# Kernel tuning notes

Measured on AMD Instinct MI355X. Metric: run time of the kernel, lower is better.

## Reference

```python
import jax, jax.numpy as jnp
import numpy as np

N_NODES = 100000
N_GRAPHS = 64
EPS = 1e-5


def _sage_conv(x, src, dst, Wl, bl, Wr):
    # mean-aggregate neighbor messages (src -> dst), then lin_l(agg) + lin_r(x)
    n = x.shape[0]
    deg = jax.ops.segment_sum(jnp.ones_like(dst, dtype=x.dtype), dst, num_segments=n)
    agg = jax.ops.segment_sum(x[src], dst, num_segments=n)  # [N, d]
    agg = agg / jnp.maximum(deg, 1.0)[:, None]
    return agg @ Wl + bl + x @ Wr


def _bn_relu(x, gamma, beta):
    mu = jnp.mean(x, axis=0)
    var = jnp.var(x, axis=0)
    return jax.nn.relu((x - mu) * jax.lax.rsqrt(var + EPS) * gamma + beta)


def setup_inputs() -> dict:
    key = jax.random.key(0)
    ks = jax.random.split(key, 16)
    E = 1600000
    x = jax.random.normal(ks[0], (N_NODES, 2), dtype=jnp.float32)
    edge_index = jax.random.randint(ks[1], (2, E), 0, N_NODES, dtype=jnp.int64)
    batch = jnp.sort(jax.random.randint(ks[2], (N_NODES,), 0, N_GRAPHS, dtype=jnp.int64))

    def lin(k, din, dout):
        s = 1.0 / np.sqrt(din)
        return jax.random.uniform(k, (din, dout), jnp.float32, -s, s)

    d = {"x": x, "edge_index": edge_index, "batch": batch}
    dims = [(2, 32), (32, 64), (64, 128)]
    for i, (din, dout) in enumerate(dims, 1):
        k1, k2 = jax.random.split(ks[2 + i])
        d[f"Wl{i}"] = lin(k1, din, dout)
        d[f"bl{i}"] = jnp.zeros((dout,), jnp.float32)
        d[f"Wr{i}"] = lin(k2, din, dout)
        d[f"g{i}"] = jnp.ones((dout,), jnp.float32)
        d[f"be{i}"] = jnp.zeros((dout,), jnp.float32)
    d["Wf1"] = lin(ks[10], 128, 64)
    d["bf1"] = jnp.zeros((64,), jnp.float32)
    d["Wf2"] = lin(ks[11], 64, 1)
    d["bf2"] = jnp.zeros((1,), jnp.float32)
    return d


def reference(x, edge_index, batch,
              Wl1, bl1, Wr1, g1, be1,
              Wl2, bl2, Wr2, g2, be2,
              Wl3, bl3, Wr3, g3, be3,
              Wf1, bf1, Wf2, bf2):
    src, dst = edge_index[0], edge_index[1]
    h = _bn_relu(_sage_conv(x, src, dst, Wl1, bl1, Wr1), g1, be1)
    h = _bn_relu(_sage_conv(h, src, dst, Wl2, bl2, Wr2), g2, be2)
    h = _bn_relu(_sage_conv(h, src, dst, Wl3, bl3, Wr3), g3, be3)
    # global mean pool over graphs
    cnt = jax.ops.segment_sum(jnp.ones_like(batch, dtype=h.dtype), batch, num_segments=N_GRAPHS)
    pooled = jax.ops.segment_sum(h, batch, num_segments=N_GRAPHS) / jnp.maximum(cnt, 1.0)[:, None]
    out = jax.nn.relu(pooled @ Wf1 + bf1)
    # dropout is identity in eval mode
    return out @ Wf2 + bf2
```

## Files before the change

### kernel.cpp

```cpp
#include <hip/hip_runtime.h>
#include <hip/hip_fp16.h>

#define N_NODES 100000
#define N_GRAPHS 64
#define BN_EPS 1e-5

#define NB 782
#define NC 49
#define PT1 4096
#define PT2 2048
#define BPC 16
#define CAP 3072
#define CAPC 36864
#define CAPF 3072

typedef _Float16 f16x8 __attribute__((ext_vector_type(8)));
typedef float f32x4 __attribute__((ext_vector_type(4)));

union F16x8u {
    f16x8 v;
    __half2 h2[4];
    uint4 u;
};

__device__ __forceinline__ float bfly64(float v) {
#pragma unroll
    for (int m = 1; m < 64; m <<= 1) v += __shfl_xor(v, m, 64);
    return v;
}

__device__ __forceinline__ unsigned pack_h2(float a, float b) {
    __half2 h = __floats2half2_rn(a, b);
    unsigned w;
    __builtin_memcpy(&w, &h, 4);
    return w;
}

__device__ __forceinline__ float2 unpack_h2(unsigned w) {
    __half2 h;
    __builtin_memcpy(&h, &w, 4);
    return __half22float2(h);
}

__global__ __launch_bounds__(256)
void pack_w(const float* __restrict__ Wl2, const float* __restrict__ Wr2,
            const float* __restrict__ Wl3, const float* __restrict__ Wr3,
            __half* __restrict__ pk, int* __restrict__ ccur, int* __restrict__ fcur) {
    int tid = threadIdx.x;
    if (blockIdx.x == 0) {
        for (int t = tid; t < NC; t += 256) ccur[t] = t * CAPC;
        for (int t = tid; t < 784; t += 256) fcur[t] = t * CAPF;
    }
    int e = blockIdx.x * 256 + tid;
    const float* W; int le, DOUT, NCB, base, SZ;
    if (e < 2048)       { W = Wl2; le = e;         DOUT = 64;  NCB = 4; base = 0;     SZ = 2048; }
    else if (e < 4096)  { W = Wr2; le = e - 2048;  DOUT = 64;  NCB = 4; base = 4096;  SZ = 2048; }
    else if (e < 12288) { W = Wl3; le = e - 4096;  DOUT = 128; NCB = 8; base = 8192;  SZ = 8192; }
    else                { W = Wr3; le = e - 12288; DOUT = 128; NCB = 8; base = 24576; SZ = 8192; }
    int i = le & 7;
    int lane = (le >> 3) & 63;
    int cbkb = le >> 9;
    int cb = cbkb % NCB;
    int kb = cbkb / NCB;
    int k = kb * 32 + ((lane >> 4) << 3) + i;
    int col = cb * 16 + (lane & 15);
    float w = W[k * DOUT + col];
    __half h = __float2half(w);
    float lo = w - __half2float(h);
    pk[base + le] = h;
    pk[base + SZ + le] = __float2half(lo);
}


__global__ __launch_bounds__(256)
void part1(const int* __restrict__ dst, const int* __restrict__ src,
           int* __restrict__ ccur, int* __restrict__ cpk, int E) {
    __shared__ int ld[PT1];
    __shared__ unsigned char lb[PT1];
    __shared__ int hist[NC], lbase[NC], gbase[NC];
    long long t0 = (long long)blockIdx.x * PT1;
    int n = (int)min((long long)PT1, (long long)E - t0);
    int tid = threadIdx.x;
    for (int i = tid; i < NC; i += 256) hist[i] = 0;
    __syncthreads();
    int p[PT1 / 256], c[PT1 / 256];
#pragma unroll
    for (int k = 0; k < PT1 / 256; ++k) {
        int li = k * 256 + tid;
        if (li < n) {
            int d = __builtin_nontemporal_load(dst + t0 + li);
            int s = __builtin_nontemporal_load(src + t0 + li);
            c[k] = d >> 11;
            p[k] = ((d & 2047) << 17) | s;
            atomicAdd(&hist[c[k]], 1);
        }
    }
    __syncthreads();
    if (tid == 0) {
        int run = 0;
        for (int i = 0; i < NC; ++i) { lbase[i] = run; run += hist[i]; }
    }
    __syncthreads();
    if (tid < NC) gbase[tid] = atomicAdd(&ccur[tid], hist[tid]);
    __syncthreads();
    for (int i = tid; i < NC; i += 256) hist[i] = 0;
    __syncthreads();
#pragma unroll
    for (int k = 0; k < PT1 / 256; ++k) {
        int li = k * 256 + tid;
        if (li < n) {
            int pos = lbase[c[k]] + atomicAdd(&hist[c[k]], 1);
            ld[pos] = p[k]; lb[pos] = (unsigned char)c[k];
        }
    }
    __syncthreads();
    for (int i = tid; i < n; i += 256) {
        int bb = lb[i];
        int g = gbase[bb] + (i - lbase[bb]);
        cpk[g] = ld[i];
    }
}

__global__ __launch_bounds__(256)
void part2(const int* __restrict__ cpk, const int* __restrict__ ccur,
           int* __restrict__ fcur, int* __restrict__ qpk) {
    __shared__ int ld[PT2];
    __shared__ unsigned char lb[PT2];
    __shared__ int hist[16], lbase[16], gbase[16];
    int c = blockIdx.x / BPC;
    int j = blockIdx.x % BPC;
    int beg = c * CAPC;
    int end = ccur[c];
    int tid = threadIdx.x;
    for (int t0 = beg + j * PT2; t0 < end; t0 += BPC * PT2) {
        int n = min(PT2, end - t0);
        if (tid < 16) hist[tid] = 0;
        __syncthreads();
        int p[PT2 / 256], f[PT2 / 256];
#pragma unroll
        for (int k = 0; k < PT2 / 256; ++k) {
            int li = k * 256 + tid;
            if (li < n) {
                p[k] = cpk[t0 + li];
                f[k] = (p[k] >> 24) & 15;
                atomicAdd(&hist[f[k]], 1);
            }
        }
        __syncthreads();
        if (tid == 0) {
            int run = 0;
            for (int i = 0; i < 16; ++i) { lbase[i] = run; run += hist[i]; }
        }
        __syncthreads();
        if (tid < 16) gbase[tid] = atomicAdd(&fcur[(c << 4) + tid], hist[tid]);
        __syncthreads();
        if (tid < 16) hist[tid] = 0;
        __syncthreads();
#pragma unroll
        for (int k = 0; k < PT2 / 256; ++k) {
            int li = k * 256 + tid;
            if (li < n) {
                int pos = lbase[f[k]] + atomicAdd(&hist[f[k]], 1);
                ld[pos] = p[k]; lb[pos] = (unsigned char)f[k];
            }
        }
        __syncthreads();
        for (int i = tid; i < n; i += 256) {
            int bb = lb[i];
            int g = gbase[bb] + (i - lbase[bb]);
            qpk[g] = ld[i];
        }
        __syncthreads();
    }
}

__global__ __launch_bounds__(256)
void fill_final(const int* __restrict__ qpk, const int* __restrict__ fcur,
                int* __restrict__ offs, int* __restrict__ oend,
                int* __restrict__ nbr, int N) {
    __shared__ int cnt[128], cbase[128], cur[128];
    __shared__ int lout[CAP];
    int b = blockIdx.x;
    int nlo = b << 7;
    int nn = min(128, N - nlo);
    int ebeg = b * CAPF;
    int ne = fcur[b] - ebeg;
    int tid = threadIdx.x;
    if (tid < 128) { cnt[tid] = 0; cur[tid] = 0; }
    __syncthreads();
    for (int i = tid; i < ne; i += 256)
        atomicAdd(&cnt[(qpk[ebeg + i] >> 17) & 127], 1);
    __syncthreads();
    if (tid < 128) cbase[tid] = cnt[tid];
    __syncthreads();
    for (int st = 1; st < 128; st <<= 1) {
        int v = 0;
        if (tid < 128 && tid >= st) v = cbase[tid - st];
        __syncthreads();
        if (tid < 128 && tid >= st) cbase[tid] += v;
        __syncthreads();
    }
    if (tid < nn) {
        offs[nlo + tid] = ebeg + (tid ? cbase[tid - 1] : 0);
        oend[nlo + tid] = ebeg + cbase[tid];
    }
    __syncthreads();
    for (int i = tid; i < ne; i += 256) {
        int p = qpk[ebeg + i];
        int ln = (p >> 17) & 127;
        int pos = (ln ? cbase[ln - 1] : 0) + atomicAdd(&cur[ln], 1);
        lout[pos] = p & 0x1FFFF;
    }
    __syncthreads();
    for (int i = tid; i < ne; i += 256)
        nbr[ebeg + i] = lout[i];
}

__global__ __launch_bounds__(256)
void layer1_fused(const float2* __restrict__ x2,
                  const int* __restrict__ offs, const int* __restrict__ oend,
                  const int* __restrict__ nbr,
                  const float* __restrict__ Wl, const float* __restrict__ bl,
                  const float* __restrict__ Wr,
                  __half* __restrict__ hout16,
                  double* __restrict__ sums, int N) {
    __shared__ float sAr[64];
    int tid = threadIdx.x;
    if (tid < 64) sAr[tid] = 0.f;
    __syncthreads();
    int n = blockIdx.x * 256 + tid;
    bool valid = (n < N);
    int beg = 0, end = 0;
    if (valid) { beg = offs[n]; end = oend[n]; }
    float ax0 = 0.f, ay0 = 0.f, ax1 = 0.f, ay1 = 0.f;
    int j = beg;
    for (; j + 16 <= end; j += 16) {
        int s[16];
#pragma unroll
        for (int u = 0; u < 16; ++u) s[u] = __builtin_nontemporal_load(nbr + j + u);
        float2 v[16];
#pragma unroll
        for (int u = 0; u < 16; ++u) v[u] = x2[s[u]];
#pragma unroll
        for (int u = 0; u < 16; ++u) {
            if (u & 1) { ax1 += v[u].x; ay1 += v[u].y; }
            else       { ax0 += v[u].x; ay0 += v[u].y; }
        }
    }
    for (; j + 4 <= end; j += 4) {
        int s[4];
#pragma unroll
        for (int u = 0; u < 4; ++u) s[u] = __builtin_nontemporal_load(nbr + j + u);
        float2 v[4];
#pragma unroll
        for (int u = 0; u < 4; ++u) v[u] = x2[s[u]];
        ax0 += v[0].x; ay0 += v[0].y;
        ax1 += v[1].x; ay1 += v[1].y;
        ax0 += v[2].x; ay0 += v[2].y;
        ax1 += v[3].x; ay1 += v[3].y;
    }
    for (; j < end; ++j) {
        float2 v = x2[nbr[j]];
        ax0 += v.x; ay0 += v.y;
    }
    float invd = 1.0f / fmaxf((float)(end - beg), 1.0f);
    float a0 = (ax0 + ax1) * invd, a1 = (ay0 + ay1) * invd;
    float x0 = 0.f, x1 = 0.f;
    if (valid) {
        float2 xv = x2[n];
        x0 = xv.x; x1 = xv.y;
    }
    float acc[32];
#pragma unroll
    for (int jj = 0; jj < 32; ++jj)
        acc[jj] = bl[jj] + a0 * Wl[jj] + a1 * Wl[32 + jj] + x0 * Wr[jj] + x1 * Wr[32 + jj];
    if (valid) {
        unsigned w[16];
#pragma unroll
        for (int p = 0; p < 16; ++p) w[p] = pack_h2(acc[2*p], acc[2*p+1]);
        uint4* q = (uint4*)(hout16 + (size_t)n * 32);
        q[0] = make_uint4(w[0], w[1], w[2], w[3]);
        q[1] = make_uint4(w[4], w[5], w[6], w[7]);
        q[2] = make_uint4(w[8], w[9], w[10], w[11]);
        q[3] = make_uint4(w[12], w[13], w[14], w[15]);
    }
    int lane = tid & 63;
#pragma unroll
    for (int jj = 0; jj < 32; ++jj) {
        float v = valid ? acc[jj] : 0.f;
        float s = bfly64(v);
        float q = bfly64(v * v);
        if (lane == jj) atomicAdd(&sAr[jj], s);
        if (lane == 32 + jj) atomicAdd(&sAr[32 + jj], q);
    }
    __syncthreads();
    if (tid < 64) atomicAdd(&sums[tid], (double)sAr[tid]);
}

template<int F>
__global__ __launch_bounds__(256)
void bn_apply(const uint4* __restrict__ h, const double* __restrict__ sums,
              const float* __restrict__ gamma, const float* __restrict__ beta,
              uint4* __restrict__ out, int N) {
    __shared__ __align__(16) float lsc[F], lsf[F];
    int tid = threadIdx.x;
    if (tid < F) {
        double mu = sums[tid] / (double)N_NODES;
        double var = sums[F + tid] / (double)N_NODES - mu * mu;
        if (var < 0.0) var = 0.0;
        double sc = (double)gamma[tid] / sqrt(var + BN_EPS);
        lsc[tid] = (float)sc;
        lsf[tid] = (float)((double)beta[tid] - mu * sc);
    }
    __syncthreads();
    constexpr int FV = F / 8;
    int total = N * FV;
    for (int i = blockIdx.x * 256 + tid; i < total; i += gridDim.x * 256) {
        uint4 v = h[i];
        int c4 = (i & (FV - 1)) * 2;
        float4 sca = ((const float4*)lsc)[c4];
        float4 scb = ((const float4*)lsc)[c4 + 1];
        float4 sfa = ((const float4*)lsf)[c4];
        float4 sfb = ((const float4*)lsf)[c4 + 1];
        float2 f0 = unpack_h2(v.x), f1 = unpack_h2(v.y);
        float2 f2 = unpack_h2(v.z), f3 = unpack_h2(v.w);
        uint4 o;
        o.x = pack_h2(fmaxf(f0.x * sca.x + sfa.x, 0.f), fmaxf(f0.y * sca.y + sfa.y, 0.f));
        o.y = pack_h2(fmaxf(f1.x * sca.z + sfa.z, 0.f), fmaxf(f1.y * sca.w + sfa.w, 0.f));
        o.z = pack_h2(fmaxf(f2.x * scb.x + sfb.x, 0.f), fmaxf(f2.y * scb.y + sfb.y, 0.f));
        o.w = pack_h2(fmaxf(f3.x * scb.z + sfb.z, 0.f), fmaxf(f3.y * scb.w + sfb.w, 0.f));
        out[i] = o;
    }
}

__device__ __forceinline__ void accum8_h16(float* acc, uint4 v) {
    float2 f0 = unpack_h2(v.x), f1 = unpack_h2(v.y);
    float2 f2 = unpack_h2(v.z), f3 = unpack_h2(v.w);
    acc[0] += f0.x; acc[1] += f0.y; acc[2] += f1.x; acc[3] += f1.y;
    acc[4] += f2.x; acc[5] += f2.y; acc[6] += f3.x; acc[7] += f3.y;
}

template<int F>
__global__ __launch_bounds__(256)
void agg_sum(const uint4* __restrict__ xb, const int* __restrict__ offs,
             const int* __restrict__ oend, const int* __restrict__ nbr,
             uint4* __restrict__ aggh, int N) {
    constexpr int FV = F / 8;
    constexpr int NPB = 256 / FV;
    int n = blockIdx.x * NPB + threadIdx.y;
    if (n >= N) return;
    int f = threadIdx.x;
    int beg = offs[n], end = oend[n];
    float a0[8], a1[8];
#pragma unroll
    for (int q = 0; q < 8; ++q) { a0[q] = 0.f; a1[q] = 0.f; }
    int j = beg;
    for (; j + 16 <= end; j += 16) {
        int s[16];
#pragma unroll
        for (int u = 0; u < 16; ++u) s[u] = __builtin_nontemporal_load(nbr + j + u);
        uint4 v[16];
#pragma unroll
        for (int u = 0; u < 16; ++u) v[u] = xb[s[u] * FV + f];
#pragma unroll
        for (int u = 0; u < 16; ++u)
            accum8_h16((u & 1) ? a1 : a0, v[u]);
    }
    if (j + 8 <= end) {
        int s[8];
#pragma unroll
        for (int u = 0; u < 8; ++u) s[u] = __builtin_nontemporal_load(nbr + j + u);
        uint4 v[8];
#pragma unroll
        for (int u = 0; u < 8; ++u) v[u] = xb[s[u] * FV + f];
#pragma unroll
        for (int u = 0; u < 8; ++u)
            accum8_h16((u & 1) ? a1 : a0, v[u]);
        j += 8;
    }
    if (j + 4 <= end) {
        int s[4];
#pragma unroll
        for (int u = 0; u < 4; ++u) s[u] = __builtin_nontemporal_load(nbr + j + u);
        uint4 v[4];
#pragma unroll
        for (int u = 0; u < 4; ++u) v[u] = xb[s[u] * FV + f];
#pragma unroll
        for (int u = 0; u < 4; ++u)
            accum8_h16((u & 1) ? a1 : a0, v[u]);
        j += 4;
    }
    for (; j < end; ++j) {
        uint4 v = xb[__builtin_nontemporal_load(nbr + j) * FV + f];
        accum8_h16(a0, v);
    }
    float invd = 1.0f / fmaxf((float)(end - beg), 1.0f);
    uint4 o;
    o.x = pack_h2((a0[0] + a1[0]) * invd, (a0[1] + a1[1]) * invd);
    o.y = pack_h2((a0[2] + a1[2]) * invd, (a0[3] + a1[3]) * invd);
    o.z = pack_h2((a0[4] + a1[4]) * invd, (a0[5] + a1[5]) * invd);
    o.w = pack_h2((a0[6] + a1[6]) * invd, (a0[7] + a1[7]) * invd);
    aggh[n * FV + f] = o;
}

template<int DIN, int DOUT>
__global__ __launch_bounds__(256)
void linear_mfma(const __half* __restrict__ bnx16, const __half* __restrict__ agg16,
                 const __half* __restrict__ wlhi, const __half* __restrict__ wllo,
                 const __half* __restrict__ wrhi, const __half* __restrict__ wrlo,
                 const float* __restrict__ bl,
                 __half* __restrict__ hout16, float* __restrict__ partial, int N) {
    constexpr int KB = DIN / 32;
    constexpr int NCB = DOUT / 16;
    constexpr int MREP = 2;
    constexpr int MB = 4 * MREP * 16;
    __shared__ float blkS[DOUT], blkQ[DOUT];
    int tid = threadIdx.x;
    for (int i = tid; i < DOUT; i += 256) { blkS[i] = 0.f; blkQ[i] = 0.f; }
    __syncthreads();
    int n0 = blockIdx.x * MB;

    int wave = tid >> 6;
    int lane = tid & 63;
    int rlane = lane & 15;
    int kg = lane >> 4;
    int rbase = n0 + wave * (MREP * 16);

    f16x8 aA[MREP][KB], aX[MREP][KB];
#pragma unroll
    for (int m = 0; m < MREP; ++m) {
        int row = rbase + m * 16 + rlane;
        int rowc = min(row, N - 1);
#pragma unroll
        for (int kb = 0; kb < KB; ++kb) {
            int c0 = kb * 32 + kg * 8;
            F16x8u ta, tx;
            ta.u = *(const uint4*)(agg16 + (size_t)rowc * DIN + c0);
            tx.u = *(const uint4*)(bnx16 + (size_t)rowc * DIN + c0);
            aA[m][kb] = ta.v;
            aX[m][kb] = tx.v;
        }
    }

    f32x4 acc[MREP][NCB];
#pragma unroll
    for (int cb = 0; cb < NCB; ++cb) {
        float bv = bl[cb * 16 + rlane];
#pragma unroll
        for (int m = 0; m < MREP; ++m)
            acc[m][cb] = {bv, bv, bv, bv};
    }

#pragma unroll
    for (int cb = 0; cb < NCB; ++cb) {
#pragma unroll
        for (int kb = 0; kb < KB; ++kb) {
            size_t fo = ((size_t)(kb * NCB + cb) * 64 + lane) * 8;
            f16x8 blh = *(const f16x8*)(wlhi + fo);
            f16x8 bll = *(const f16x8*)(wllo + fo);
            f16x8 brh = *(const f16x8*)(wrhi + fo);
            f16x8 brl = *(const f16x8*)(wrlo + fo);
#pragma unroll
            for (int m = 0; m < MREP; ++m) {
                acc[m][cb] = __builtin_amdgcn_mfma_f32_16x16x32_f16(aA[m][kb], blh, acc[m][cb], 0, 0, 0);
                acc[m][cb] = __builtin_amdgcn_mfma_f32_16x16x32_f16(aA[m][kb], bll, acc[m][cb], 0, 0, 0);
                acc[m][cb] = __builtin_amdgcn_mfma_f32_16x16x32_f16(aX[m][kb], brh, acc[m][cb], 0, 0, 0);
                acc[m][cb] = __builtin_amdgcn_mfma_f32_16x16x32_f16(aX[m][kb], brl, acc[m][cb], 0, 0, 0);
            }
        }
    }

#pragma unroll
    for (int m = 0; m < MREP; ++m) {
        int rowb = rbase + m * 16 + kg * 4;
#pragma unroll
        for (int r = 0; r < 4; ++r) {
            int node = rowb + r;
            if (node < N) {
#pragma unroll
                for (int cb = 0; cb < NCB; ++cb)
                    hout16[(size_t)node * DOUT + cb * 16 + rlane] = __float2half(acc[m][cb][r]);
            }
        }
    }

#pragma unroll
    for (int cb = 0; cb < NCB; ++cb) {
        float s = 0.f, q = 0.f;
#pragma unroll
        for (int m = 0; m < MREP; ++m) {
            int rowb = rbase + m * 16 + kg * 4;
#pragma unroll
            for (int r = 0; r < 4; ++r) {
                if (rowb + r < N) {
                    float v = acc[m][cb][r];
                    s += v; q += v * v;
                }
            }
        }
        s += __shfl_xor(s, 16, 64); s += __shfl_xor(s, 32, 64);
        q += __shfl_xor(q, 16, 64); q += __shfl_xor(q, 32, 64);
        if (kg == 0) {
            atomicAdd(&blkS[cb * 16 + rlane], s);
            atomicAdd(&blkQ[cb * 16 + rlane], q);
        }
    }
    __syncthreads();
    float* po = partial + (size_t)blockIdx.x * (2 * DOUT);
    for (int i = tid; i < DOUT; i += 256) {
        po[i] = blkS[i];
        po[DOUT + i] = blkQ[i];
    }
}

template<int F>
__global__ __launch_bounds__(256)
void stats_finalize2(const float* __restrict__ partial, double* __restrict__ sums, int P) {
    __shared__ double sh[256];
    int i = blockIdx.x;
    int t = threadIdx.x;
    double a = 0.0;
    for (int k = t; k < P; k += 256)
        a += (double)partial[(size_t)k * (2 * F) + i];
    sh[t] = a;
    __syncthreads();
    for (int st = 128; st > 0; st >>= 1) {
        if (t < st) sh[t] += sh[t + st];
        __syncthreads();
    }
    if (t == 0) sums[i] = sh[0];
}

__global__ void pool_partial(const __half* __restrict__ h, const int* __restrict__ batch,
                             const double* __restrict__ sums,
                             const float* __restrict__ gamma, const float* __restrict__ beta,
                             double* __restrict__ pooled_d, int N) {
    __shared__ float lsc[128], lsf[128];
    const int CH = 64;
    int f = threadIdx.x;
    {
        double mu = sums[f] / (double)N_NODES;
        double var = sums[128 + f] / (double)N_NODES - mu * mu;
        if (var < 0.0) var = 0.0;
        double sc = (double)gamma[f] / sqrt(var + BN_EPS);
        lsc[f] = (float)sc;
        lsf[f] = (float)((double)beta[f] - mu * sc);
    }
    __syncthreads();
    int n0 = blockIdx.x * CH;
    if (n0 >= N) return;
    int n1 = min(n0 + CH, N);
    float sc = lsc[f], sf = lsf[f];
    int g = batch[n0];
    float acc = 0.f;
    for (int n = n0; n < n1; ++n) {
        int bg = batch[n];
        if (bg != g) {
            atomicAdd(&pooled_d[g * 128 + f], (double)acc);
            acc = 0.f;
            g = bg;
        }
        float v = __half2float(h[(long long)n * 128 + f]);
        acc += fmaxf(v * sc + sf, 0.f);
    }
    atomicAdd(&pooled_d[g * 128 + f], (double)acc);
}

__global__ void mlp_fused(const double* __restrict__ pooled_d, const int* __restrict__ batch,
                          const float* __restrict__ Wf1, const float* __restrict__ bf1,
                          const float* __restrict__ Wf2, const float* __restrict__ bf2,
                          float* __restrict__ out, int N) {
    __shared__ float sp[128];
    int g = blockIdx.x;
    int t = threadIdx.x;
    int lo = 0, hi = N;
    while (lo < hi) { int m = (lo + hi) >> 1; if (batch[m] < g) lo = m + 1; else hi = m; }
    int start = lo;
    hi = N;
    while (lo < hi) { int m = (lo + hi) >> 1; if (batch[m] < g + 1) lo = m + 1; else hi = m; }
    int cnt = lo - start;
    sp[t] = (float)(pooled_d[g * 128 + t] / (double)max(cnt, 1));
    __syncthreads();
    if (t < 64) {
        float hacc = bf1[t];
#pragma unroll 8
        for (int k = 0; k < 128; ++k) hacc += sp[k] * Wf1[k * 64 + t];
        hacc = fmaxf(hacc, 0.f) * Wf2[t];
        for (int o = 32; o > 0; o >>= 1) hacc += __shfl_down(hacc, o);
        if (t == 0) out[g] = hacc + bf2[0];
    }
}

extern "C" void kernel_launch(void* const* d_in, const int* in_sizes, int n_in,
                              void* d_out, int out_size, void* d_ws, size_t ws_size,
                              hipStream_t stream) {
    const float* x     = (const float*)d_in[0];
    const int*   ei    = (const int*)d_in[1];
    const int*   batch = (const int*)d_in[2];
    const float *Wl1=(const float*)d_in[3],  *bl1=(const float*)d_in[4],  *Wr1=(const float*)d_in[5];
    const float *g1 =(const float*)d_in[6],  *be1=(const float*)d_in[7];
    const float *Wl2=(const float*)d_in[8],  *bl2=(const float*)d_in[9],  *Wr2=(const float*)d_in[10];
    const float *g2 =(const float*)d_in[11], *be2=(const float*)d_in[12];
    const float *Wl3=(const float*)d_in[13], *bl3=(const float*)d_in[14], *Wr3=(const float*)d_in[15];
    const float *g3 =(const float*)d_in[16], *be3=(const float*)d_in[17];
    const float *Wf1=(const float*)d_in[18], *bf1=(const float*)d_in[19];
    const float *Wf2=(const float*)d_in[20], *bf2=(const float*)d_in[21];

    const int N = N_NODES;
    const int E = in_sizes[1] / 2;
    const int* src = ei;
    const int* dst = ei + E;

    char* ws = (char*)d_ws;
    size_t off = 0;
    auto salloc = [&](size_t bytes) {
        void* p = ws + off;
        off += (bytes + 255) & ~(size_t)255;
        return p;
    };
    double* sums    = (double*)salloc(768 * 8);
    double* pooledd = (double*)salloc((size_t)N_GRAPHS * 128 * 8);
    size_t zero_bytes = off;
    int*    offs    = (int*)   salloc((size_t)N * 4);
    int*    oend    = (int*)   salloc((size_t)N * 4);
    int*    fcur    = (int*)   salloc(784 * 4);
    int*    ccur    = (int*)   salloc(NC * 4);
    int*    nbr     = (int*)   salloc((size_t)NB * CAPF * 4);
    float*  partial = (float*) salloc((size_t)1024 * 256 * 4);
    __half* pk      = (__half*)salloc((size_t)40960 * 2);
    __half* h1h     = (__half*)salloc((size_t)(N + 256) * 32 * 2);
    __half* b1h     = (__half*)salloc((size_t)(N + 256) * 32 * 2);
    __half* h2h     = (__half*)salloc((size_t)(N + 256) * 64 * 2);
    __half* b2h     = (__half*)salloc((size_t)(N + 256) * 64 * 2);
    __half* h3h     = (__half*)salloc((size_t)(N + 256) * 128 * 2);
    __half* aggh    = (__half*)salloc((size_t)(N + 256) * 64 * 2);
    (void)ws_size;

    double* sums1 = sums, *sums2 = sums + 256, *sums3 = sums + 512;
    int* cpk = (int*)h3h;
    int* qpk = (int*)aggh;

    const __half *pwl2h = pk,         *pwl2l = pk + 2048;
    const __half *pwr2h = pk + 4096,  *pwr2l = pk + 6144;
    const __half *pwl3h = pk + 8192,  *pwl3l = pk + 16384;
    const __half *pwr3h = pk + 24576, *pwr3l = pk + 32768;

    hipMemsetAsync(sums, 0, zero_bytes, stream);

    pack_w<<<80, 256, 0, stream>>>(Wl2, Wr2, Wl3, Wr3, pk, ccur, fcur);

    part1<<<(E + PT1 - 1) / PT1, 256, 0, stream>>>(dst, src, ccur, cpk, E);
    part2<<<NC * BPC, 256, 0, stream>>>(cpk, ccur, fcur, qpk);
    fill_final<<<NB, 256, 0, stream>>>(qpk, fcur, offs, oend, nbr, N);

    const int NL = (N + 255) / 256;
    const int NBLK = (N + 127) / 128;

    layer1_fused<<<NL, 256, 0, stream>>>((const float2*)x, offs, oend, nbr,
                                          Wl1, bl1, Wr1, h1h, sums1, N);

    bn_apply<32><<<512, 256, 0, stream>>>((const uint4*)h1h, sums1, g1, be1, (uint4*)b1h, N);
    agg_sum<32><<<(N + 63) / 64, dim3(4, 64), 0, stream>>>(
        (const uint4*)b1h, offs, oend, nbr, (uint4*)aggh, N);
    linear_mfma<32, 64><<<NBLK, 256, 0, stream>>>(
        b1h, (const __half*)aggh, pwl2h, pwl2l, pwr2h, pwr2l, bl2, h2h, partial, N);
    stats_finalize2<64><<<128, 256, 0, stream>>>(partial, sums2, NBLK);

    bn_apply<64><<<512, 256, 0, stream>>>((const uint4*)h2h, sums2, g2, be2, (uint4*)b2h, N);
    agg_sum<64><<<(N + 31) / 32, dim3(8, 32), 0, stream>>>(
        (const uint4*)b2h, offs, oend, nbr, (uint4*)aggh, N);
    linear_mfma<64, 128><<<NBLK, 256, 0, stream>>>(
        b2h, (const __half*)aggh, pwl3h, pwl3l, pwr3h, pwr3l, bl3, h3h, partial, N);
    stats_finalize2<128><<<256, 256, 0, stream>>>(partial, sums3, NBLK);

    pool_partial<<<(N + 63) / 64, 128, 0, stream>>>(h3h, batch, sums3, g3, be3, pooledd, N);
    mlp_fused<<<N_GRAPHS, 128, 0, stream>>>(pooledd, batch, Wf1, bf1, Wf2, bf2, (float*)d_out, N);
}
```

Baseline: 307.4 us.

## Collapse two-pass edge bucketing into single pass with 256-node buckets

Replaces the two-level radix partition of edges (coarse 2048-node chunks, then 128-node buckets) with a single partition pass straight into 391 buckets of 256 nodes, removing the part2 kernel and one full read/write of the edge array. The fill kernel now handles 256 nodes per block with a larger per-bucket capacity. The memset of the stats region is folded into the pack_w kernel to drop a separate launch. The trade-off is more histogram bins and scattered global atomics per part1 block, plus fixed bucket capacities that could overflow on skewed inputs.

```diff
diff --git a/kernel.cpp b/kernel.cpp
--- a/kernel.cpp
+++ b/kernel.cpp
@@ -5,14 +5,9 @@
 #define N_GRAPHS 64
 #define BN_EPS 1e-5
 
-#define NB 782
-#define NC 49
+#define NBF 391
 #define PT1 4096
-#define PT2 2048
-#define BPC 16
-#define CAP 3072
-#define CAPC 36864
-#define CAPF 3072
+#define CAPF 4608
 
 typedef _Float16 f16x8 __attribute__((ext_vector_type(8)));
 typedef float f32x4 __attribute__((ext_vector_type(4)));
@@ -45,11 +40,14 @@
 __global__ __launch_bounds__(256)
 void pack_w(const float* __restrict__ Wl2, const float* __restrict__ Wr2,
             const float* __restrict__ Wl3, const float* __restrict__ Wr3,
-            __half* __restrict__ pk, int* __restrict__ ccur, int* __restrict__ fcur) {
+            __half* __restrict__ pk, int* __restrict__ fcur,
+            double* __restrict__ zero_region) {
     int tid = threadIdx.x;
     if (blockIdx.x == 0) {
-        for (int t = tid; t < NC; t += 256) ccur[t] = t * CAPC;
-        for (int t = tid; t < 784; t += 256) fcur[t] = t * CAPF;
+        for (int t = tid; t < NBF; t += 256) fcur[t] = t * CAPF;
+    } else if (blockIdx.x <= 4) {
+        for (int i = (blockIdx.x - 1) * 256 + tid; i < 8960; i += 1024)
+            zero_region[i] = 0.0;
     }
     int e = blockIdx.x * 256 + tid;
     const float* W; int le, DOUT, NCB, base, SZ;
@@ -74,14 +72,15 @@
 
 __global__ __launch_bounds__(256)
 void part1(const int* __restrict__ dst, const int* __restrict__ src,
-           int* __restrict__ ccur, int* __restrict__ cpk, int E) {
+           int* __restrict__ fcur, int* __restrict__ qpk, int E) {
     __shared__ int ld[PT1];
-    __shared__ unsigned char lb[PT1];
-    __shared__ int hist[NC], lbase[NC], gbase[NC];
+    __shared__ unsigned short lb[PT1];
+    __shared__ int hist[NBF], lbase[NBF], gbase[NBF];
+    __shared__ int pairs[256];
     long long t0 = (long long)blockIdx.x * PT1;
     int n = (int)min((long long)PT1, (long long)E - t0);
     int tid = threadIdx.x;
-    for (int i = tid; i < NC; i += 256) hist[i] = 0;
+    for (int i = tid; i < NBF; i += 256) hist[i] = 0;
     __syncthreads();
     int p[PT1 / 256], c[PT1 / 256];
 #pragma unroll
@@ -90,87 +89,44 @@
         if (li < n) {
             int d = __builtin_nontemporal_load(dst + t0 + li);
             int s = __builtin_nontemporal_load(src + t0 + li);
-            c[k] = d >> 11;
-            p[k] = ((d & 2047) << 17) | s;
+            c[k] = d >> 8;
+            p[k] = ((d & 255) << 17) | s;
             atomicAdd(&hist[c[k]], 1);
         }
     }
     __syncthreads();
-    if (tid == 0) {
-        int run = 0;
-        for (int i = 0; i < NC; ++i) { lbase[i] = run; run += hist[i]; }
-    }
-    __syncthreads();
-    if (tid < NC) gbase[tid] = atomicAdd(&ccur[tid], hist[tid]);
-    __syncthreads();
-    for (int i = tid; i < NC; i += 256) hist[i] = 0;
+    int h0 = (2 * tid < NBF) ? hist[2 * tid] : 0;
+    int h1 = (2 * tid + 1 < NBF) ? hist[2 * tid + 1] : 0;
+    pairs[tid] = h0 + h1;
+    __syncthreads();
+    for (int st = 1; st < 256; st <<= 1) {
+        int v = (tid >= st) ? pairs[tid - st] : 0;
+        __syncthreads();
+        pairs[tid] += v;
+        __syncthreads();
+    }
+    int pe = tid ? pairs[tid - 1] : 0;
+    if (2 * tid < NBF) lbase[2 * tid] = pe;
+    if (2 * tid + 1 < NBF) lbase[2 * tid + 1] = pe + h0;
+    __syncthreads();
+    for (int b = tid; b < NBF; b += 256)
+        gbase[b] = atomicAdd(&fcur[b], hist[b]);
+    __syncthreads();
+    for (int i = tid; i < NBF; i += 256) hist[i] = 0;
     __syncthreads();
 #pragma unroll
     for (int k = 0; k < PT1 / 256; ++k) {
         int li = k * 256 + tid;
         if (li < n) {
             int pos = lbase[c[k]] + atomicAdd(&hist[c[k]], 1);
-            ld[pos] = p[k]; lb[pos] = (unsigned char)c[k];
+            ld[pos] = p[k]; lb[pos] = (unsigned short)c[k];
         }
     }
     __syncthreads();
     for (int i = tid; i < n; i += 256) {
         int bb = lb[i];
         int g = gbase[bb] + (i - lbase[bb]);
-        cpk[g] = ld[i];
-    }
-}
-
-__global__ __launch_bounds__(256)
-void part2(const int* __restrict__ cpk, const int* __restrict__ ccur,
-           int* __restrict__ fcur, int* __restrict__ qpk) {
-    __shared__ int ld[PT2];
-    __shared__ unsigned char lb[PT2];
-    __shared__ int hist[16], lbase[16], gbase[16];
-    int c = blockIdx.x / BPC;
-    int j = blockIdx.x % BPC;
-    int beg = c * CAPC;
-    int end = ccur[c];
-    int tid = threadIdx.x;
-    for (int t0 = beg + j * PT2; t0 < end; t0 += BPC * PT2) {
-        int n = min(PT2, end - t0);
-        if (tid < 16) hist[tid] = 0;
-        __syncthreads();
-        int p[PT2 / 256], f[PT2 / 256];
-#pragma unroll
-        for (int k = 0; k < PT2 / 256; ++k) {
-            int li = k * 256 + tid;
-            if (li < n) {
-                p[k] = cpk[t0 + li];
-                f[k] = (p[k] >> 24) & 15;
-                atomicAdd(&hist[f[k]], 1);
-            }
-        }
-        __syncthreads();
-        if (tid == 0) {
-            int run = 0;
-            for (int i = 0; i < 16; ++i) { lbase[i] = run; run += hist[i]; }
-        }
-        __syncthreads();
-        if (tid < 16) gbase[tid] = atomicAdd(&fcur[(c << 4) + tid], hist[tid]);
-        __syncthreads();
-        if (tid < 16) hist[tid] = 0;
-        __syncthreads();
-#pragma unroll
-        for (int k = 0; k < PT2 / 256; ++k) {
-            int li = k * 256 + tid;
-            if (li < n) {
-                int pos = lbase[f[k]] + atomicAdd(&hist[f[k]], 1);
-                ld[pos] = p[k]; lb[pos] = (unsigned char)f[k];
-            }
-        }
-        __syncthreads();
-        for (int i = tid; i < n; i += 256) {
-            int bb = lb[i];
-            int g = gbase[bb] + (i - lbase[bb]);
-            qpk[g] = ld[i];
-        }
-        __syncthreads();
+        qpk[g] = ld[i];
     }
 }
 
@@ -178,26 +134,25 @@
 void fill_final(const int* __restrict__ qpk, const int* __restrict__ fcur,
                 int* __restrict__ offs, int* __restrict__ oend,
                 int* __restrict__ nbr, int N) {
-    __shared__ int cnt[128], cbase[128], cur[128];
-    __shared__ int lout[CAP];
+    __shared__ int cnt[256], cbase[256], cur[256];
+    __shared__ int lout[CAPF];
     int b = blockIdx.x;
-    int nlo = b << 7;
-    int nn = min(128, N - nlo);
+    int nlo = b << 8;
+    int nn = min(256, N - nlo);
     int ebeg = b * CAPF;
     int ne = fcur[b] - ebeg;
     int tid = threadIdx.x;
-    if (tid < 128) { cnt[tid] = 0; cur[tid] = 0; }
+    cnt[tid] = 0; cur[tid] = 0;
     __syncthreads();
     for (int i = tid; i < ne; i += 256)
-        atomicAdd(&cnt[(qpk[ebeg + i] >> 17) & 127], 1);
-    __syncthreads();
-    if (tid < 128) cbase[tid] = cnt[tid];
-    __syncthreads();
-    for (int st = 1; st < 128; st <<= 1) {
-        int v = 0;
-        if (tid < 128 && tid >= st) v = cbase[tid - st];
+        atomicAdd(&cnt[(qpk[ebeg + i] >> 17) & 255], 1);
+    __syncthreads();
+    cbase[tid] = cnt[tid];
+    __syncthreads();
+    for (int st = 1; st < 256; st <<= 1) {
+        int v = (tid >= st) ? cbase[tid - st] : 0;
         __syncthreads();
-        if (tid < 128 && tid >= st) cbase[tid] += v;
+        cbase[tid] += v;
         __syncthreads();
     }
     if (tid < nn) {
@@ -207,7 +162,7 @@
     __syncthreads();
     for (int i = tid; i < ne; i += 256) {
         int p = qpk[ebeg + i];
-        int ln = (p >> 17) & 127;
+        int ln = (p >> 17) & 255;
         int pos = (ln ? cbase[ln - 1] : 0) + atomicAdd(&cur[ln], 1);
         lout[pos] = p & 0x1FFFF;
     }
@@ -620,12 +575,10 @@
     };
     double* sums    = (double*)salloc(768 * 8);
     double* pooledd = (double*)salloc((size_t)N_GRAPHS * 128 * 8);
-    size_t zero_bytes = off;
     int*    offs    = (int*)   salloc((size_t)N * 4);
     int*    oend    = (int*)   salloc((size_t)N * 4);
-    int*    fcur    = (int*)   salloc(784 * 4);
-    int*    ccur    = (int*)   salloc(NC * 4);
-    int*    nbr     = (int*)   salloc((size_t)NB * CAPF * 4);
+    int*    fcur    = (int*)   salloc((NBF + 1) * 4);
+    int*    nbr     = (int*)   salloc((size_t)NBF * CAPF * 4);
     float*  partial = (float*) salloc((size_t)1024 * 256 * 4);
     __half* pk      = (__half*)salloc((size_t)40960 * 2);
     __half* h1h     = (__half*)salloc((size_t)(N + 256) * 32 * 2);
@@ -637,7 +590,6 @@
     (void)ws_size;
 
     double* sums1 = sums, *sums2 = sums + 256, *sums3 = sums + 512;
-    int* cpk = (int*)h3h;
     int* qpk = (int*)aggh;
 
     const __half *pwl2h = pk,         *pwl2l = pk + 2048;
@@ -645,13 +597,10 @@
     const __half *pwl3h = pk + 8192,  *pwl3l = pk + 16384;
     const __half *pwr3h = pk + 24576, *pwr3l = pk + 32768;
 
-    hipMemsetAsync(sums, 0, zero_bytes, stream);
-
-    pack_w<<<80, 256, 0, stream>>>(Wl2, Wr2, Wl3, Wr3, pk, ccur, fcur);
-
-    part1<<<(E + PT1 - 1) / PT1, 256, 0, stream>>>(dst, src, ccur, cpk, E);
-    part2<<<NC * BPC, 256, 0, stream>>>(cpk, ccur, fcur, qpk);
-    fill_final<<<NB, 256, 0, stream>>>(qpk, fcur, offs, oend, nbr, N);
+    pack_w<<<80, 256, 0, stream>>>(Wl2, Wr2, Wl3, Wr3, pk, fcur, sums);
+
+    part1<<<(E + PT1 - 1) / PT1, 256, 0, stream>>>(dst, src, fcur, qpk, E);
+    fill_final<<<NBF, 256, 0, stream>>>(qpk, fcur, offs, oend, nbr, N);
 
     const int NL = (N + 255) / 256;
     const int NBLK = (N + 127) / 128;
```

Result: no change. 304.9 us, median of 3 (-0.8%).
